# Kernel tuning notes

Hardware: AMD Instinct MI355X
Metric: run time of the kernel (lower is better)

The kernel has to match this reference:

```python
import jax, jax.numpy as jnp
import numpy as np

EMBED_DIM = 1024
LATENT = 512
HEADS = 8
HEAD_DIM = EMBED_DIM // HEADS        # 128
LAT_HD = LATENT // HEADS             # 64
EPS = 1e-5


def _layernorm(x, gamma, beta):
    mu = jnp.mean(x, axis=-1, keepdims=True)
    var = jnp.mean(jnp.square(x - mu), axis=-1, keepdims=True)
    return (x - mu) * jax.lax.rsqrt(var + EPS) * gamma + beta


def setup_inputs() -> dict:
    key = jax.random.key(0)
    ks = jax.random.split(key, 12)
    B, N, M = 8, 8192, 256
    s_in = 1.0 / np.sqrt(EMBED_DIM)
    return {
        "input_tokens": jax.random.normal(ks[0], (B, N, EMBED_DIM), jnp.float32),
        "query_tokens": jax.random.normal(ks[1], (B, M, EMBED_DIM), jnp.float32),
        # Linear weights stored as [in, out] so y = x @ W + b
        "q_w": jax.random.normal(ks[2], (EMBED_DIM, LATENT), jnp.float32) * s_in,
        "q_b": jnp.zeros((LATENT,), jnp.float32),
        "q_g": jnp.ones((LATENT,), jnp.float32),
        "q_beta": jnp.zeros((LATENT,), jnp.float32),
        "k_w": jax.random.normal(ks[3], (EMBED_DIM, LATENT), jnp.float32) * s_in,
        "k_b": jnp.zeros((LATENT,), jnp.float32),
        "k_g": jnp.ones((LATENT,), jnp.float32),
        "k_beta": jnp.zeros((LATENT,), jnp.float32),
        "v_w": jax.random.normal(ks[4], (EMBED_DIM, EMBED_DIM), jnp.float32) * s_in,
        "v_b": jnp.zeros((EMBED_DIM,), jnp.float32),
        "v_g": jnp.ones((EMBED_DIM,), jnp.float32),
        "v_beta": jnp.zeros((EMBED_DIM,), jnp.float32),
        "proj_w": jax.random.normal(ks[5], (EMBED_DIM, EMBED_DIM), jnp.float32) * s_in,
        "proj_b": jnp.zeros((EMBED_DIM,), jnp.float32),
    }


def reference(input_tokens, query_tokens, q_w, q_b, q_g, q_beta,
              k_w, k_b, k_g, k_beta, v_w, v_b, v_g, v_beta,
              proj_w, proj_b):
    B, N, C = input_tokens.shape
    M = query_tokens.shape[1]
    # projections + layernorms
    q = _layernorm(query_tokens @ q_w + q_b, q_g, q_beta)   # [B,M,LATENT]
    k = _layernorm(input_tokens @ k_w + k_b, k_g, k_beta)   # [B,N,LATENT]
    v = _layernorm(input_tokens @ v_w + v_b, v_g, v_beta)   # [B,N,C]
    # split heads: q,k -> [B,H,*,LAT_HD]; v -> [B,H,N,HEAD_DIM]
    q = q.reshape(B, M, HEADS, LAT_HD).transpose(0, 2, 1, 3)
    k = k.reshape(B, N, HEADS, LAT_HD).transpose(0, 2, 1, 3)
    v = v.reshape(B, N, HEADS, HEAD_DIM).transpose(0, 2, 1, 3)
    # softmax Q over latent head dim; softmax K^T over token dim N
    q = jax.nn.softmax(q, axis=-1)                 # [B,H,M,LAT_HD]
    kT = jax.nn.softmax(k.transpose(0, 1, 3, 2), axis=-1)  # [B,H,LAT_HD,N]
    kv = jnp.einsum('bhln,bhnd->bhld', kT, v)      # [B,H,LAT_HD,HEAD_DIM]
    out = jnp.einsum('bhml,bhld->bhmd', q, kv)     # [B,H,M,HEAD_DIM]
    out = out.transpose(0, 2, 1, 3).reshape(B, M, C)
    return out @ proj_w + proj_b
```

## Files before the change

kernel.cpp:

```cpp
#include <hip/hip_runtime.h>
#include <hip/hip_fp16.h>

typedef _Float16 f16;
typedef _Float16 f16x8 __attribute__((ext_vector_type(8)));
typedef _Float16 f16x4 __attribute__((ext_vector_type(4)));
typedef float f32x4 __attribute__((ext_vector_type(4)));

#define LN_EPS 1e-5f

typedef __attribute__((address_space(1))) unsigned int as1_u32;
typedef __attribute__((address_space(3))) unsigned int as3_u32;

__device__ __forceinline__ void gload_lds16(const void* g, void* l) {
    __builtin_amdgcn_global_load_lds((as1_u32*)g, (as3_u32*)l, 16, 0, 0);
}

__device__ __forceinline__ f32x4 mfma16(f16x8 a, f16x8 b, f32x4 c) {
    return __builtin_amdgcn_mfma_f32_16x16x32_f16(a, b, c, 0, 0, 0);
}


__global__ void k_cvt_dual(const float4* __restrict__ in0, const float4* __restrict__ in1,
                           f16x4* __restrict__ out0, f16x4* __restrict__ out1,
                           int nsplit, int ntot) {
    int i = blockIdx.x * blockDim.x + threadIdx.x;
    int st = gridDim.x * blockDim.x;
    for (; i < ntot; i += st) {
        const bool lo = i < nsplit;
        const float4 v = lo ? in0[i] : in1[i - nsplit];
        f16x4 o;
        o.x = (f16)v.x; o.y = (f16)v.y; o.z = (f16)v.z; o.w = (f16)v.w;
        if (lo) out0[i] = o; else out1[i - nsplit] = o;
    }
}

__global__ __launch_bounds__(256) void k_transpose_all(const float* __restrict__ kw,
                                                       const float* __restrict__ vw,
                                                       const float* __restrict__ qw,
                                                       const float* __restrict__ pw,
                                                       f16* __restrict__ BkvT,
                                                       f16* __restrict__ qwT,
                                                       f16* __restrict__ pwT) {
    __shared__ float t[32][33];
    const int x = blockIdx.x;
    const float* W; f16* WT; int Nw, nt0;
    if (x < 16)      { W = kw; WT = BkvT;                     Nw = 512;  nt0 = x; }
    else if (x < 48) { W = vw; WT = BkvT + (size_t)512 * 1024; Nw = 1024; nt0 = x - 16; }
    else if (x < 64) { W = qw; WT = qwT;                      Nw = 512;  nt0 = x - 48; }
    else             { W = pw; WT = pwT;                      Nw = 1024; nt0 = x - 64; }
    const int n0 = nt0 * 32, k0 = blockIdx.y * 32;
    const int tx = threadIdx.x & 31, ty = threadIdx.x >> 5;
#pragma unroll
    for (int i = 0; i < 32; i += 8)
        t[ty + i][tx] = W[(size_t)(k0 + ty + i) * Nw + n0 + tx];
    __syncthreads();
#pragma unroll
    for (int i = 0; i < 32; i += 8)
        WT[(size_t)(n0 + ty + i) * 1024 + k0 + tx] = (f16)t[tx][ty + i];
}


__global__ __launch_bounds__(512, 2) void k_gemm256(const f16* __restrict__ A,
                                                    const f16* __restrict__ Bt,
                                                    f16* __restrict__ C,
                                                    const float* __restrict__ bias1,
                                                    const float* __restrict__ bias2,
                                                    float* __restrict__ stats) {
    extern __shared__ char lds[];
    const int tid = threadIdx.x, lane = tid & 63, w = tid >> 6;
    const int wr = w >> 2, wc = w & 3;
    const int lane15 = lane & 15, l4 = lane >> 4;

    const int swz = ((int)blockIdx.x & 7) * 192 + ((int)blockIdx.x >> 3);
    const int bx = swz % 6, by = swz / 6;
    const size_t m0 = (size_t)by * 256, n0g = (size_t)bx * 256;

    const int lrow4 = lane >> 2;
    const int lchunk = (lane & 3) ^ ((lane >> 3) & 3);
    const f16* gA = A + (m0 + w * 32 + lrow4) * 1024 + lchunk * 8;
    const f16* gB = Bt + (n0g + w * 32 + lrow4) * 1024 + lchunk * 8;
    const int dstA = w * 2048;

    const int csw = l4 ^ ((lane15 >> 1) & 3);
    const int ofsA = (wr * 128 + lane15) * 64 + csw * 16;
    const int ofsB = 16384 + (wc * 64 + lane15) * 64 + csw * 16;

    f32x4 acc[8][4] = {};

#define STAGE_C(content)                                                         \
    {                                                                            \
        const int _sl = (content) & 3;                                           \
        const int _ko = ((content) >> 1) * 64 + ((content) & 1) * 32;            \
        char* _b = lds + _sl * 32768;                                            \
        gload_lds16(gA + _ko, _b + dstA);                                        \
        gload_lds16(gA + _ko + 16 * 1024, _b + dstA + 1024);                     \
        gload_lds16(gB + _ko, _b + 16384 + dstA);                                \
        gload_lds16(gB + _ko + 16 * 1024, _b + 16384 + dstA + 1024);             \
    }

#define PHASE(slotc, stage_content, vmN)                                         \
    {                                                                            \
        const char* sb = lds + (slotc) * 32768;                                  \
        f16x8 af[8], bf[4];                                                      \
        _Pragma("unroll") for (int m = 0; m < 8; m++)                            \
            af[m] = *(const f16x8*)(sb + ofsA + m * 1024);                       \
        _Pragma("unroll") for (int n = 0; n < 4; n++)                            \
            bf[n] = *(const f16x8*)(sb + ofsB + n * 1024);                       \
        if ((stage_content) >= 0) STAGE_C(stage_content)                         \
        if ((vmN) == 8) asm volatile("s_waitcnt vmcnt(8)" ::: "memory");         \
        else if ((vmN) == 4) asm volatile("s_waitcnt vmcnt(4)" ::: "memory");    \
        else if ((vmN) == 0) asm volatile("s_waitcnt vmcnt(0)" ::: "memory");    \
        __builtin_amdgcn_s_barrier();                                            \
        __builtin_amdgcn_s_setprio(1);                                           \
        _Pragma("unroll") for (int m = 0; m < 8; m++)                            \
            _Pragma("unroll") for (int n = 0; n < 4; n++)                        \
                acc[m][n] = mfma16(af[m], bf[n], acc[m][n]);                     \
        __builtin_amdgcn_s_setprio(0);                                           \
        __builtin_amdgcn_s_barrier();                                            \
    }

    STAGE_C(0) STAGE_C(1) STAGE_C(2)
    asm volatile("s_waitcnt vmcnt(8)" ::: "memory");
    __builtin_amdgcn_s_barrier();

#pragma unroll 4
    for (int g = 0; g < 28; ++g) PHASE(g & 3, g + 3, 8)
    PHASE(0, 31, 8)
    PHASE(1, -1, 4)
    PHASE(2, -1, 0)
    PHASE(3, -1, -1)
#undef PHASE
#undef STAGE_C

    {
        f16* Ct = (f16*)lds;
#pragma unroll
        for (int m = 0; m < 8; m++)
#pragma unroll
            for (int n = 0; n < 4; n++) {
                const int row = wr * 128 + m * 16 + l4 * 4;
                const int col = wc * 64 + n * 16 + lane15;
                const int cg = (int)n0g + col;
                const float bv = (cg < 512) ? bias1[cg] : bias2[cg - 512];
#pragma unroll
                for (int j = 0; j < 4; j++)
                    Ct[(row + j) * 256 + col] = (f16)(acc[m][n][j] + bv);
            }
        __syncthreads();
#pragma unroll
        for (int it = 0; it < 16; it++) {
            const int flat = it * 512 + tid;
            const int row = flat >> 5;
            const int ce = (flat & 31) * 8;
            *(f16x8*)(C + (m0 + row) * 1536 + n0g + ce) = *(const f16x8*)(Ct + row * 256 + ce);
        }
        __syncthreads();
    }
    {
        float* SP = (float*)lds;
        const int part = (n0g >= 512) ? 1 : 0;
#pragma unroll
        for (int half = 0; half < 2; half++) {
            float s1[4][4], s2[4][4];
#pragma unroll
            for (int m = 0; m < 4; m++)
#pragma unroll
                for (int j = 0; j < 4; j++) { s1[m][j] = 0.f; s2[m][j] = 0.f; }
#pragma unroll
            for (int m = 0; m < 4; m++) {
                const int mm = half * 4 + m;
#pragma unroll
                for (int n = 0; n < 4; n++) {
                    const int cg = (int)n0g + wc * 64 + n * 16 + lane15;
                    const float bv = (cg < 512) ? bias1[cg] : bias2[cg - 512];
#pragma unroll
                    for (int j = 0; j < 4; j++) {
                        const float v = acc[mm][n][j] + bv;
                        s1[m][j] += v;
                        s2[m][j] += v * v;
                    }
                }
#pragma unroll
                for (int j = 0; j < 4; j++) {
#pragma unroll
                    for (int o = 1; o < 16; o <<= 1) {
                        s1[m][j] += __shfl_xor(s1[m][j], o);
                        s2[m][j] += __shfl_xor(s2[m][j], o);
                    }
                }
            }
            if (lane15 == 0) {
#pragma unroll
                for (int m = 0; m < 4; m++)
#pragma unroll
                    for (int j = 0; j < 4; j++) {
                        const int row = wr * 128 + (half * 4 + m) * 16 + l4 * 4 + j;
                        SP[row * 8 + wc * 2 + 0] = s1[m][j];
                        SP[row * 8 + wc * 2 + 1] = s2[m][j];
                    }
            }
        }
        __syncthreads();
        {
            const int row = tid >> 1, comp = tid & 1;
            const float v = SP[row * 8 + 0 + comp] + SP[row * 8 + 2 + comp] +
                            SP[row * 8 + 4 + comp] + SP[row * 8 + 6 + comp];
            atomicAdd(stats + (m0 + row) * 4 + part * 2 + comp, v);
        }
    }
}

__global__ void k_statsfin(float4* __restrict__ stats) {
    const int i = blockIdx.x * 256 + threadIdx.x;
    const float4 s = stats[i];
    const float muk = s.x * (1.f / 512.f);
    const float vk = s.y * (1.f / 512.f) - muk * muk;
    const float muv = s.z * (1.f / 1024.f);
    const float vv = s.w * (1.f / 1024.f) - muv * muv;
    stats[i] = make_float4(muk, rsqrtf(vk + LN_EPS), muv, rsqrtf(vv + LN_EPS));
}


template <bool OUTF32>
__global__ __launch_bounds__(256, 2) void k_gemm(const f16* __restrict__ A,
                                                 const f16* __restrict__ Bt,
                                                 void* __restrict__ Cout, int Ncols, int Kd,
                                                 const float* __restrict__ bias1,
                                                 const float* __restrict__ bias2, int bsplit) {
    __shared__ f16 smem[16384];
    const int tid = threadIdx.x, lane = tid & 63, wave = tid >> 6;
    const int m0 = blockIdx.y * 128, n0 = blockIdx.x * 128;
    const size_t ldb = (size_t)Kd * 2;
    f32x4 acc[4][4] = {};

    const int rA = wave * 8 + (lane >> 3);
    const int slot = (lane & 7) * 16;
    const char* Ab = (const char*)A + (size_t)(m0 + rA) * ldb + slot;
    const char* Bb = (const char*)Bt + (size_t)(n0 + rA) * ldb + slot;
    char* lA = (char*)smem + wave * 1024;
    char* lB = (char*)smem + 16384 + wave * 1024;

    const int wm = (wave & 1) * 64, wn = (wave >> 1) * 64;

    for (int k0 = 0; k0 < Kd; k0 += 64) {
#pragma unroll
        for (int i = 0; i < 4; i++) {
            gload_lds16(Ab + (size_t)k0 * 2 + (size_t)i * 32 * ldb, lA + i * 4096);
            gload_lds16(Bb + (size_t)k0 * 2 + (size_t)i * 32 * ldb, lB + i * 4096);
        }
        __syncthreads();
#pragma unroll
        for (int kk = 0; kk < 64; kk += 32) {
            const int kb = (kk + (lane >> 4) * 8) * 2;
            f16x8 af[4], bf[4];
#pragma unroll
            for (int mi = 0; mi < 4; mi++)
                af[mi] = *(const f16x8*)((const char*)smem + (wm + mi * 16 + (lane & 15)) * 128 + kb);
#pragma unroll
            for (int ni = 0; ni < 4; ni++)
                bf[ni] = *(const f16x8*)((const char*)smem + 16384 + (wn + ni * 16 + (lane & 15)) * 128 + kb);
#pragma unroll
            for (int mi = 0; mi < 4; mi++)
#pragma unroll
                for (int ni = 0; ni < 4; ni++)
                    acc[mi][ni] = mfma16(af[mi], bf[ni], acc[mi][ni]);
        }
        __syncthreads();
    }

    if (!OUTF32) {
        f16* Ct = smem;
#pragma unroll
        for (int mi = 0; mi < 4; mi++) {
#pragma unroll
            for (int ni = 0; ni < 4; ni++) {
                const int r = wm + mi * 16 + (lane >> 4) * 4;
                const int c = wn + ni * 16 + (lane & 15);
                const int cg = n0 + c;
                const float bv = (cg < bsplit) ? bias1[cg] : bias2[cg - bsplit];
#pragma unroll
                for (int j = 0; j < 4; j++) Ct[(r + j) * 128 + c] = (f16)(acc[mi][ni][j] + bv);
            }
        }
        __syncthreads();
        f16* Cg = (f16*)Cout;
        const int r = tid >> 1, half = tid & 1;
        const f16* src = Ct + r * 128 + half * 64;
        f16* dst = Cg + (size_t)(m0 + r) * Ncols + n0 + half * 64;
#pragma unroll
        for (int i = 0; i < 8; i++) *(f16x8*)(dst + i * 8) = *(const f16x8*)(src + i * 8);
    } else {
        float* Cg = (float*)Cout;
#pragma unroll
        for (int mi = 0; mi < 4; mi++) {
#pragma unroll
            for (int ni = 0; ni < 4; ni++) {
                const int r = wm + mi * 16 + (lane >> 4) * 4;
                const int c = wn + ni * 16 + (lane & 15);
                const int cg = n0 + c;
                const float bv = (cg < bsplit) ? bias1[cg] : bias2[cg - bsplit];
#pragma unroll
                for (int j = 0; j < 4; j++)
                    Cg[(size_t)(m0 + r + j) * Ncols + cg] = acc[mi][ni][j] + bv;
            }
        }
    }
}


__global__ __launch_bounds__(256) void k_colstats1(const f16* __restrict__ Ckv,
                                                   const float4* __restrict__ stats,
                                                   const float* __restrict__ kg,
                                                   const float* __restrict__ kb,
                                                   float* __restrict__ pm, float* __restrict__ ps) {
    const int b = blockIdx.y, slab = blockIdx.x, t = threadIdx.x;
    const int c0 = t * 2;
    const float g0 = kg[c0], g1 = kg[c0 + 1], e0 = kb[c0], e1 = kb[c0 + 1];
    const size_t r0 = (size_t)b * 8192 + slab * 64;
    float m0 = -1e30f, m1 = -1e30f;
    for (int r = 0; r < 64; r++) {
        const float4 st = stats[r0 + r];
        union { unsigned u; f16 h[2]; } w;
        w.u = *(const unsigned*)(Ckv + (r0 + r) * 1536 + c0);
        const float z0 = ((float)w.h[0] - st.x) * st.y * g0 + e0;
        const float z1 = ((float)w.h[1] - st.x) * st.y * g1 + e1;
        m0 = fmaxf(m0, z0);
        m1 = fmaxf(m1, z1);
    }
    float s0 = 0.f, s1 = 0.f;
    for (int r = 0; r < 64; r++) {
        const float4 st = stats[r0 + r];
        union { unsigned u; f16 h[2]; } w;
        w.u = *(const unsigned*)(Ckv + (r0 + r) * 1536 + c0);
        const float z0 = ((float)w.h[0] - st.x) * st.y * g0 + e0;
        const float z1 = ((float)w.h[1] - st.x) * st.y * g1 + e1;
        s0 += __expf(z0 - m0);
        s1 += __expf(z1 - m1);
    }
    const int o = (b * 128 + slab) * 512 + c0;
    pm[o] = m0; pm[o + 1] = m1;
    ps[o] = s0; ps[o + 1] = s1;
}

__global__ void k_colstats2(const float* __restrict__ pm, const float* __restrict__ ps,
                            float* __restrict__ Mx, float* __restrict__ invZ) {
    const int idx = blockIdx.x * 256 + threadIdx.x;
    const int b = idx >> 9, c = idx & 511;
    float M = -1e30f;
    for (int s = 0; s < 128; s++) M = fmaxf(M, pm[(b * 128 + s) * 512 + c]);
    float S = 0.f;
    for (int s = 0; s < 128; s++) S += ps[(b * 128 + s) * 512 + c] * __expf(pm[(b * 128 + s) * 512 + c] - M);
    Mx[idx] = M;
    invZ[idx] = 1.0f / S;
}


__global__ __launch_bounds__(256, 2) void k_kv(const f16* __restrict__ Ckv,
                                               const float4* __restrict__ stats,
                                               const float* __restrict__ kg,
                                               const float* __restrict__ kbe,
                                               const float* __restrict__ vg,
                                               const float* __restrict__ vbe,
                                               const float* __restrict__ Mx,
                                               float* __restrict__ kvpart) {
    __shared__ f16 As[64 * 64];
    __shared__ f16 Vs[128 * 64];
    __shared__ float cgk[64], cbk[64], cmx[64], cgv[128], cbv[128];
    const int split = blockIdx.x, bh = blockIdx.y;
    const int b = bh >> 3, h = bh & 7;
    const int tid = threadIdx.x, lane = tid & 63, wave = tid >> 6;
    if (tid < 64) {
        cgk[tid] = kg[h * 64 + tid];
        cbk[tid] = kbe[h * 64 + tid];
        cmx[tid] = Mx[b * 512 + h * 64 + tid];
    }
    if (tid < 128) {
        cgv[tid] = vg[h * 128 + tid];
        cbv[tid] = vbe[h * 128 + tid];
    }
    __syncthreads();
    f32x4 acc[8] = {};
    const size_t base = (size_t)b * 8192 + split * 1024;
    for (int t0 = 0; t0 < 1024; t0 += 64) {
        {
            const int g = tid & 7, p = tid >> 3;
            const size_t row = base + t0 + 2 * p;
            const f16x8 x0 = *(const f16x8*)(Ckv + row * 1536 + h * 64 + g * 8);
            const f16x8 x1 = *(const f16x8*)(Ckv + (row + 1) * 1536 + h * 64 + g * 8);
            const float4 s0 = stats[row], s1 = stats[row + 1];
#pragma unroll
            for (int j = 0; j < 8; j++) {
                const int c = g * 8 + j;
                const float z0 = ((float)x0[j] - s0.x) * s0.y * cgk[c] + cbk[c] - cmx[c];
                const float z1 = ((float)x1[j] - s1.x) * s1.y * cgk[c] + cbk[c] - cmx[c];
                union { unsigned u; f16 h2[2]; } pk;
                pk.h2[0] = (f16)__expf(z0);
                pk.h2[1] = (f16)__expf(z1);
                *(unsigned*)((char*)As + c * 128 + 4 * p) = pk.u;
            }
        }
#pragma unroll
        for (int sub = 0; sub < 2; sub++) {
            const int idx = tid + sub * 256;
            const int g = idx & 15, p = idx >> 4;
            const size_t row = base + t0 + 2 * p;
            const f16x8 x0 = *(const f16x8*)(Ckv + row * 1536 + 512 + h * 128 + g * 8);
            const f16x8 x1 = *(const f16x8*)(Ckv + (row + 1) * 1536 + 512 + h * 128 + g * 8);
            const float4 s0 = stats[row], s1 = stats[row + 1];
#pragma unroll
            for (int j = 0; j < 8; j++) {
                const int d = g * 8 + j;
                const float z0 = ((float)x0[j] - s0.z) * s0.w * cgv[d] + cbv[d];
                const float z1 = ((float)x1[j] - s1.z) * s1.w * cgv[d] + cbv[d];
                union { unsigned u; f16 h2[2]; } pk;
                pk.h2[0] = (f16)z0;
                pk.h2[1] = (f16)z1;
                *(unsigned*)((char*)Vs + d * 128 + 4 * p) = pk.u;
            }
        }
        __syncthreads();
#pragma unroll
        for (int kk = 0; kk < 64; kk += 32) {
            const int kb2 = (kk + (lane >> 4) * 8) * 2;
            const f16x8 af = *(const f16x8*)((const char*)As + (wave * 16 + (lane & 15)) * 128 + kb2);
#pragma unroll
            for (int ni = 0; ni < 8; ni++) {
                const f16x8 bf = *(const f16x8*)((const char*)Vs + (ni * 16 + (lane & 15)) * 128 + kb2);
                acc[ni] = mfma16(af, bf, acc[ni]);
            }
        }
        __syncthreads();
    }
    float* out = kvpart + ((size_t)split * 64 + bh) * 8192;
    const int l = wave * 16 + (lane >> 4) * 4;
#pragma unroll
    for (int ni = 0; ni < 8; ni++) {
        const int d = ni * 16 + (lane & 15);
#pragma unroll
        for (int j = 0; j < 4; j++) out[(l + j) * 128 + d] = acc[ni][j];
    }
}

__global__ void k_kvreduce(const float* __restrict__ kvpart, const float* __restrict__ invZ,
                           f16* __restrict__ kvT) {
    const int idx = blockIdx.x * 256 + threadIdx.x;
    const int d = idx & 127, l = (idx >> 7) & 63, bh = idx >> 13;
    const int b = bh >> 3, h = bh & 7;
    float s = 0.f;
#pragma unroll
    for (int sp = 0; sp < 8; sp++) s += kvpart[((size_t)sp * 64 + bh) * 8192 + l * 128 + d];
    s *= invZ[b * 512 + h * 64 + l];
    kvT[((size_t)bh * 128 + d) * 64 + l] = (f16)s;
}


__global__ __launch_bounds__(512) void k_qsm(const f16* __restrict__ qlin,
                                             const float* __restrict__ qg,
                                             const float* __restrict__ qbeta,
                                             f16* __restrict__ qsm) {
    const int row = blockIdx.x, t = threadIdx.x;
    const float x = (float)qlin[(size_t)row * 512 + t];
    float s = x, s2 = x * x;
#pragma unroll
    for (int off = 32; off; off >>= 1) {
        s += __shfl_xor(s, off);
        s2 += __shfl_xor(s2, off);
    }
    __shared__ float rs[16];
    const int wave = t >> 6, lane = t & 63;
    if (lane == 0) {
        rs[wave] = s;
        rs[8 + wave] = s2;
    }
    __syncthreads();
    float S = 0.f, S2 = 0.f;
#pragma unroll
    for (int w = 0; w < 8; w++) {
        S += rs[w];
        S2 += rs[8 + w];
    }
    const float mu = S * (1.0f / 512.0f);
    const float var = S2 * (1.0f / 512.0f) - mu * mu;
    const float z = (x - mu) * rsqrtf(var + LN_EPS) * qg[t] + qbeta[t];
    float m = z;
#pragma unroll
    for (int off = 32; off; off >>= 1) m = fmaxf(m, __shfl_xor(m, off));
    const float e = __expf(z - m);
    float se = e;
#pragma unroll
    for (int off = 32; off; off >>= 1) se += __shfl_xor(se, off);
    qsm[(size_t)row * 512 + t] = (f16)(e / se);
}


__global__ __launch_bounds__(256) void k_qkv(const f16* __restrict__ qsm,
                                             const f16* __restrict__ kvT,
                                             f16* __restrict__ omid) {
    const int ms = blockIdx.x, bh = blockIdx.y;
    const int b = bh >> 3, h = bh & 7;
    const int tid = threadIdx.x, lane = tid & 63, wave = tid >> 6;
    const int mr = ms * 64 + wave * 16;
    f32x4 acc[8] = {};
    const f16* Ab = qsm + (size_t)(b * 256 + mr + (lane & 15)) * 512 + h * 64;
    const f16* Bb = kvT + (size_t)bh * 8192;
#pragma unroll
    for (int kk = 0; kk < 64; kk += 32) {
        const int k = kk + (lane >> 4) * 8;
        const f16x8 af = *(const f16x8*)(Ab + k);
#pragma unroll
        for (int ni = 0; ni < 8; ni++) {
            const f16x8 bf = *(const f16x8*)(Bb + (ni * 16 + (lane & 15)) * 64 + k);
            acc[ni] = mfma16(af, bf, acc[ni]);
        }
    }
    const int r = b * 256 + mr + (lane >> 4) * 4;
#pragma unroll
    for (int ni = 0; ni < 8; ni++) {
        const int d = h * 128 + ni * 16 + (lane & 15);
#pragma unroll
        for (int j = 0; j < 4; j++) omid[(size_t)(r + j) * 1024 + d] = (f16)acc[ni][j];
    }
}


extern "C" void kernel_launch(void* const* d_in, const int* in_sizes, int n_in,
                              void* d_out, int out_size, void* d_ws, size_t ws_size,
                              hipStream_t stream) {
    const float* input  = (const float*)d_in[0];
    const float* query  = (const float*)d_in[1];
    const float* q_w    = (const float*)d_in[2];
    const float* q_b    = (const float*)d_in[3];
    const float* q_g    = (const float*)d_in[4];
    const float* q_beta = (const float*)d_in[5];
    const float* k_w    = (const float*)d_in[6];
    const float* k_b    = (const float*)d_in[7];
    const float* k_g    = (const float*)d_in[8];
    const float* k_beta = (const float*)d_in[9];
    const float* v_w    = (const float*)d_in[10];
    const float* v_b    = (const float*)d_in[11];
    const float* v_g    = (const float*)d_in[12];
    const float* v_beta = (const float*)d_in[13];
    const float* proj_w = (const float*)d_in[14];
    const float* proj_b = (const float*)d_in[15];

    char* ws = (char*)d_ws;
    size_t off = 0;
    auto alloc = [&](size_t bytes) {
        char* p = ws + off;
        off += (bytes + 255) & ~(size_t)255;
        return p;
    };
    f16*   A16    = (f16*)alloc((size_t)67108864 * 2);
    f16*   Q16    = (f16*)alloc((size_t)2097152 * 2);
    f16*   BkvT   = (f16*)alloc((size_t)1536 * 1024 * 2);
    f16*   qwT    = (f16*)alloc((size_t)512 * 1024 * 2);
    f16*   pwT    = (f16*)alloc((size_t)1024 * 1024 * 2);
    f16*   Ckv    = (f16*)alloc((size_t)65536 * 1536 * 2);
    float* stats  = (float*)alloc((size_t)65536 * 16);
    float* pm     = (float*)alloc((size_t)8 * 128 * 512 * 4);
    float* ps     = (float*)alloc((size_t)8 * 128 * 512 * 4);
    float* Mx     = (float*)alloc((size_t)8 * 512 * 4);
    float* invZ   = (float*)alloc((size_t)8 * 512 * 4);
    f16*   qlin   = (f16*)alloc((size_t)2048 * 512 * 2);
    f16*   qsm    = (f16*)alloc((size_t)2048 * 512 * 2);
    float* kvpart = (float*)alloc((size_t)8 * 64 * 64 * 128 * 4);
    f16*   kvT    = (f16*)alloc((size_t)64 * 128 * 64 * 2);
    f16*   omid   = (f16*)alloc((size_t)2048 * 1024 * 2);
    (void)ws_size; (void)in_sizes; (void)n_in; (void)out_size;

    hipFuncSetAttribute(reinterpret_cast<const void*>(k_gemm256),
                        hipFuncAttributeMaxDynamicSharedMemorySize, 131072);

    hipMemsetAsync(stats, 0, (size_t)65536 * 16, stream);

    k_cvt_dual<<<2048, 256, 0, stream>>>((const float4*)input, (const float4*)query,
                                         (f16x4*)A16, (f16x4*)Q16, 16777216, 17301504);
    k_transpose_all<<<dim3(96, 32), 256, 0, stream>>>(k_w, v_w, q_w, proj_w, BkvT, qwT, pwT);

    k_gemm256<<<1536, 512, 131072, stream>>>(A16, BkvT, Ckv, k_b, v_b, stats);
    k_statsfin<<<256, 256, 0, stream>>>((float4*)stats);

    k_colstats1<<<dim3(128, 8), 256, 0, stream>>>(Ckv, (const float4*)stats, k_g, k_beta, pm, ps);
    k_colstats2<<<16, 256, 0, stream>>>(pm, ps, Mx, invZ);

    k_kv<<<dim3(8, 64), 256, 0, stream>>>(Ckv, (const float4*)stats, k_g, k_beta, v_g, v_beta, Mx, kvpart);
    k_kvreduce<<<2048, 256, 0, stream>>>(kvpart, invZ, kvT);

    k_gemm<false><<<dim3(4, 16), 256, 0, stream>>>(Q16, qwT, qlin, 512, 1024, q_b, q_b, 512);
    k_qsm<<<2048, 512, 0, stream>>>(qlin, q_g, q_beta, qsm);
    k_qkv<<<dim3(4, 64), 256, 0, stream>>>(qsm, kvT, omid);
    k_gemm<true><<<dim3(8, 16), 256, 0, stream>>>(omid, pwT, d_out, 1024, 1024, proj_b, proj_b, 2048);
}
```

Measured before the change: 898.0 us.

## Restructure GEMM main loop to 64-wide K tiles with double-buffered staging

The fused projection GEMM main loop now uses 64-element K tiles held in two 64KB LDS buffers instead of four 32-wide slots. Each tile is consumed in four MQ sub-phases that reuse cached B fragments across A row-pairs. Global-to-LDS staging is spread across the phases, and the LDS chunk swizzle is changed to an 8-way XOR. The aim is fewer barriers per K step, more MFMAs per barrier and better B-fragment reuse. In exchange it uses 128KB of LDS, which may limit occupancy under the 2-blocks launch bound, and a more intricate wait/stage schedule.

```diff
diff --git a/kernel.cpp b/kernel.cpp
--- a/kernel.cpp
+++ b/kernel.cpp
@@ -69,68 +69,79 @@
     extern __shared__ char lds[];
     const int tid = threadIdx.x, lane = tid & 63, w = tid >> 6;
     const int wr = w >> 2, wc = w & 3;
-    const int lane15 = lane & 15, l4 = lane >> 4;
+    const int l15 = lane & 15, l4 = lane >> 4;
 
     const int swz = ((int)blockIdx.x & 7) * 192 + ((int)blockIdx.x >> 3);
     const int bx = swz % 6, by = swz / 6;
     const size_t m0 = (size_t)by * 256, n0g = (size_t)bx * 256;
 
-    const int lrow4 = lane >> 2;
-    const int lchunk = (lane & 3) ^ ((lane >> 3) & 3);
-    const f16* gA = A + (m0 + w * 32 + lrow4) * 1024 + lchunk * 8;
-    const f16* gB = Bt + (n0g + w * 32 + lrow4) * 1024 + lchunk * 8;
-    const int dstA = w * 2048;
-
-    const int csw = l4 ^ ((lane15 >> 1) & 3);
-    const int ofsA = (wr * 128 + lane15) * 64 + csw * 16;
-    const int ofsB = 16384 + (wc * 64 + lane15) * 64 + csw * 16;
+    const int srow = w * 16 + (lane >> 3);
+    const int schunk = (lane & 7) ^ (lane >> 3);
+    const f16* sA = A + (m0 + srow) * 1024 + schunk * 8;
+    const f16* sB = Bt + (n0g + srow) * 1024 + schunk * 8;
+    char* const ldsw = lds + w * 2048;
+
+    const int p0off = ((l4 ^ (l15 & 7))) * 16;
+    const int p1off = (((4 | l4) ^ (l15 & 7))) * 16;
+    const char* fA = lds + wr * 16384 + l15 * 128;
+    const char* fB = lds + (2 + (wc >> 1)) * 16384 + ((wc & 1) * 64 + l15) * 128;
 
     f32x4 acc[8][4] = {};
-
-#define STAGE_C(content)                                                         \
-    {                                                                            \
-        const int _sl = (content) & 3;                                           \
-        const int _ko = ((content) >> 1) * 64 + ((content) & 1) * 32;            \
-        char* _b = lds + _sl * 32768;                                            \
-        gload_lds16(gA + _ko, _b + dstA);                                        \
-        gload_lds16(gA + _ko + 16 * 1024, _b + dstA + 1024);                     \
-        gload_lds16(gB + _ko, _b + 16384 + dstA);                                \
-        gload_lds16(gB + _ko + 16 * 1024, _b + 16384 + dstA + 1024);             \
-    }
-
-#define PHASE(slotc, stage_content, vmN)                                         \
-    {                                                                            \
-        const char* sb = lds + (slotc) * 32768;                                  \
-        f16x8 af[8], bf[4];                                                      \
-        _Pragma("unroll") for (int m = 0; m < 8; m++)                            \
-            af[m] = *(const f16x8*)(sb + ofsA + m * 1024);                       \
-        _Pragma("unroll") for (int n = 0; n < 4; n++)                            \
-            bf[n] = *(const f16x8*)(sb + ofsB + n * 1024);                       \
-        if ((stage_content) >= 0) STAGE_C(stage_content)                         \
-        if ((vmN) == 8) asm volatile("s_waitcnt vmcnt(8)" ::: "memory");         \
-        else if ((vmN) == 4) asm volatile("s_waitcnt vmcnt(4)" ::: "memory");    \
-        else if ((vmN) == 0) asm volatile("s_waitcnt vmcnt(0)" ::: "memory");    \
-        __builtin_amdgcn_s_barrier();                                            \
-        __builtin_amdgcn_s_setprio(1);                                           \
-        _Pragma("unroll") for (int m = 0; m < 8; m++)                            \
-            _Pragma("unroll") for (int n = 0; n < 4; n++)                        \
-                acc[m][n] = mfma16(af[m], bf[n], acc[m][n]);                     \
-        __builtin_amdgcn_s_setprio(0);                                           \
-        __builtin_amdgcn_s_barrier();                                            \
-    }
-
-    STAGE_C(0) STAGE_C(1) STAGE_C(2)
-    asm volatile("s_waitcnt vmcnt(8)" ::: "memory");
+    f16x8 bfr[4][2];
+
+#define STG(kt, part, isB, j)                                                      \
+    gload_lds16(((isB) ? sB : sA) + ((part) * 128 + (j) * 8) * 1024 + ((kt) & 15) * 64, \
+                ldsw + ((((kt) & 1) * 4 + ((isB) ? 2 : 0) + (part)) * 16384) + (j) * 1024)
+#define STG2(kt, part, isB) { STG(kt, part, isB, 0); STG(kt, part, isB, 1); }
+
+#define PHASE(PAR, MQ, VM, STAGES)                                                 \
+    {                                                                              \
+        if (MQ == 0) {                                                             \
+            _Pragma("unroll") for (int n = 0; n < 4; n++) {                        \
+                bfr[n][0] = *(const f16x8*)(fB + (PAR)*65536 + n * 2048 + p0off);  \
+                bfr[n][1] = *(const f16x8*)(fB + (PAR)*65536 + n * 2048 + p1off);  \
+            }                                                                      \
+        }                                                                          \
+        f16x8 a0k0 = *(const f16x8*)(fA + (PAR)*65536 + (MQ * 2) * 2048 + p0off);  \
+        f16x8 a0k1 = *(const f16x8*)(fA + (PAR)*65536 + (MQ * 2) * 2048 + p1off);  \
+        f16x8 a1k0 = *(const f16x8*)(fA + (PAR)*65536 + (MQ * 2 + 1) * 2048 + p0off); \
+        f16x8 a1k1 = *(const f16x8*)(fA + (PAR)*65536 + (MQ * 2 + 1) * 2048 + p1off); \
+        STAGES;                                                                    \
+        if ((VM) >= 0) asm volatile("s_waitcnt vmcnt(4)" ::: "memory");            \
+        __builtin_amdgcn_s_barrier();                                              \
+        __builtin_amdgcn_s_setprio(1);                                             \
+        _Pragma("unroll") for (int n = 0; n < 4; n++) {                            \
+            acc[MQ * 2][n] = mfma16(a0k0, bfr[n][0], acc[MQ * 2][n]);              \
+            acc[MQ * 2][n] = mfma16(a0k1, bfr[n][1], acc[MQ * 2][n]);              \
+            acc[MQ * 2 + 1][n] = mfma16(a1k0, bfr[n][0], acc[MQ * 2 + 1][n]);      \
+            acc[MQ * 2 + 1][n] = mfma16(a1k1, bfr[n][1], acc[MQ * 2 + 1][n]);      \
+        }                                                                          \
+        __builtin_amdgcn_s_setprio(0);                                             \
+        __builtin_amdgcn_s_barrier();                                              \
+    }
+
+    STG2(0, 0, 1) STG2(0, 1, 1) STG2(0, 0, 0) STG2(0, 1, 0) STG2(1, 0, 1) STG2(1, 1, 1)
+    asm volatile("s_waitcnt vmcnt(4)" ::: "memory");
     __builtin_amdgcn_s_barrier();
 
-#pragma unroll 4
-    for (int g = 0; g < 28; ++g) PHASE(g & 3, g + 3, 8)
-    PHASE(0, 31, 8)
-    PHASE(1, -1, 4)
-    PHASE(2, -1, 0)
-    PHASE(3, -1, -1)
+#pragma unroll 1
+    for (int i = 0; i < 8; i++) {
+        const int t1 = 2 * i + 1, t2 = 2 * i + 2, t3 = 2 * i + 3;
+        PHASE(0, 0, -1, STG2(t1, 0, 0))
+        PHASE(0, 1, -1, STG2(t1, 1, 0); STG2(t2, 0, 1))
+        PHASE(0, 2, -1, STG2(t2, 1, 1))
+        PHASE(0, 3, 4, (void)0)
+        PHASE(1, 0, -1, STG2(t2, 0, 0))
+        PHASE(1, 1, -1, STG2(t2, 1, 0); STG2(t3, 0, 1))
+        PHASE(1, 2, -1, STG2(t3, 1, 1))
+        PHASE(1, 3, 4, (void)0)
+    }
 #undef PHASE
-#undef STAGE_C
+#undef STG2
+#undef STG
+
+    asm volatile("s_waitcnt vmcnt(0)" ::: "memory");
+    __syncthreads();
 
     {
         f16* Ct = (f16*)lds;
@@ -139,7 +150,7 @@
 #pragma unroll
             for (int n = 0; n < 4; n++) {
                 const int row = wr * 128 + m * 16 + l4 * 4;
-                const int col = wc * 64 + n * 16 + lane15;
+                const int col = wc * 64 + n * 16 + l15;
                 const int cg = (int)n0g + col;
                 const float bv = (cg < 512) ? bias1[cg] : bias2[cg - 512];
 #pragma unroll
@@ -171,7 +182,7 @@
                 const int mm = half * 4 + m;
 #pragma unroll
                 for (int n = 0; n < 4; n++) {
-                    const int cg = (int)n0g + wc * 64 + n * 16 + lane15;
+                    const int cg = (int)n0g + wc * 64 + n * 16 + l15;
                     const float bv = (cg < 512) ? bias1[cg] : bias2[cg - 512];
 #pragma unroll
                     for (int j = 0; j < 4; j++) {
@@ -189,7 +200,7 @@
                     }
                 }
             }
-            if (lane15 == 0) {
+            if (l15 == 0) {
 #pragma unroll
                 for (int m = 0; m < 4; m++)
 #pragma unroll
```

Measured after the change: 880.0 us. 2.0% less time.
